# Kernel optimization log

Measured on AMD Instinct MI355X. Metric: run time of the kernel, lower is better.

Reference implementation:

```python
import jax, jax.numpy as jnp
import numpy as np

WH, WW = 7, 7
N = WH * WW
H = 16          # num_heads
D = 32          # head_dim
NW = 64         # num windows per image (mask.shape[0])


def _relative_position_index(wh, ww):
    coords = np.stack(np.meshgrid(np.arange(wh), np.arange(ww), indexing='ij'))  # (2, wh, ww)
    cf = coords.reshape(2, -1)                                                   # (2, N)
    rel = cf[:, :, None] - cf[:, None, :]                                        # (2, N, N)
    rel = rel.transpose(1, 2, 0).copy()
    rel[:, :, 0] += wh - 1
    rel[:, :, 1] += ww - 1
    rel[:, :, 0] *= 2 * ww - 1
    return rel.sum(-1)  # (N, N) int

REL_IDX = jnp.asarray(_relative_position_index(WH, WW))


def setup_inputs() -> dict:
    key = jax.random.key(0)
    ks = jax.random.split(key, 5)
    B_ = 2048
    dim = H * D
    x = jax.random.normal(ks[0], (B_, N, dim), dtype=jnp.float32)
    mask = jnp.zeros((NW, N, N), dtype=jnp.float32)
    rpb_table = jax.random.normal(ks[1], ((2 * WH - 1) * (2 * WW - 1), H), dtype=jnp.float32) * 0.02
    qkv_w = jax.random.normal(ks[2], (3 * dim, dim), dtype=jnp.float32) * (dim ** -0.5)
    qkv_b = jnp.zeros((3 * dim,), dtype=jnp.float32)
    proj_w = jax.random.normal(ks[3], (dim, dim), dtype=jnp.float32) * (dim ** -0.5)
    proj_b = jnp.zeros((dim,), dtype=jnp.float32)
    return {"x": x, "mask": mask, "rpb_table": rpb_table,
            "qkv_w": qkv_w, "qkv_b": qkv_b, "proj_w": proj_w, "proj_b": proj_b}


def reference(x, mask, rpb_table, qkv_w, qkv_b, proj_w, proj_b):
    B_, n, C = x.shape
    scale = D ** -0.5
    # qkv projection (torch Linear: x @ W^T + b)
    qkv = (x @ qkv_w.T + qkv_b).reshape(B_, n, 3, H, D)
    q = qkv[:, :, 0].transpose(0, 2, 1, 3) * scale  # (B_, H, N, D)
    k = qkv[:, :, 1].transpose(0, 2, 1, 3)
    v = qkv[:, :, 2].transpose(0, 2, 1, 3)
    attn = jnp.einsum('bhnd,bhmd->bhnm', q, k)      # (B_, H, N, N)
    # relative position bias: gather (N*N,) rows from table -> (N, N, H) -> (H, N, N)
    bias = rpb_table[REL_IDX.reshape(-1)].reshape(n, n, H).transpose(2, 0, 1)
    attn = attn + bias[None]
    # shifted-window mask add: (B, nW, H, N, N) + (1, nW, 1, N, N)
    nW = mask.shape[0]
    attn = attn.reshape(B_ // nW, nW, H, n, n) + mask[None, :, None]
    attn = attn.reshape(B_, H, n, n)
    attn = jax.nn.softmax(attn, axis=-1)
    out = jnp.einsum('bhnm,bhmd->bhnd', attn, v)    # (B_, H, N, D)
    out = out.transpose(0, 2, 1, 3).reshape(B_, n, H * D)
    return out @ proj_w.T + proj_b
```

## Files before the change

### kernel.cpp

```cpp
#include <hip/hip_runtime.h>

typedef _Float16 f16;
typedef _Float16 f16x8 __attribute__((ext_vector_type(8)));
typedef _Float16 f16x4 __attribute__((ext_vector_type(4)));
typedef float f32x4 __attribute__((ext_vector_type(4)));

#define NTOK 49
#define NH 16
#define HD 32
#define DIM 512
#define NWIN 64
#define NB 2048
#define MTOT (NB*NTOK)
#define SCALE 0.17677669529663687f
#define VTS 56

__device__ __forceinline__ void gload_lds16(const f16* g, f16* l) {
    __builtin_amdgcn_global_load_lds((const __attribute__((address_space(1))) void*)g,
                                     (__attribute__((address_space(3))) void*)l, 16, 0, 0);
}

__global__ __launch_bounds__(256) void cvt_f32_f16(const float* __restrict__ s,
                                                   f16* __restrict__ d, int n4) {
    int i = blockIdx.x * 256 + threadIdx.x;
    int st = gridDim.x * 256;
    for (; i < n4; i += st) {
        float4 v = ((const float4*)s)[i];
        f16x4 o = { (f16)v.x, (f16)v.y, (f16)v.z, (f16)v.w };
        *(f16x4*)(d + (size_t)i * 4) = o;
    }
}

__global__ __launch_bounds__(256) void build_comb2(const float* __restrict__ rpb,
                                                   const float* __restrict__ mask,
                                                   float* __restrict__ comb2) {
    int idx = blockIdx.x * 256 + threadIdx.x;
    int r4   = idx & 3;
    int tj   = (idx >> 2) & 3;
    int ti   = (idx >> 4) & 3;
    int lane = (idx >> 6) & 63;
    int wh   = idx >> 12;
    int h = wh & 15, w = wh >> 4;
    int g = lane >> 4, c16 = lane & 15;
    int row = ti * 16 + g * 4 + r4;
    int col = tj * 16 + c16;
    float v = 0.f;
    if (row < NTOK && col < NTOK) {
        int ri = row / 7, ci = row - ri * 7;
        int rj = col / 7, cj = col - rj * 7;
        int rel = (ri - rj + 6) * 13 + (ci - cj + 6);
        v = rpb[rel * NH + h] + mask[(w * NTOK + row) * NTOK + col];
    }
    comb2[idx] = v;
}

template<int MODE, int NT>
__global__ __launch_bounds__(256, 3) void gemm_kernel(const f16* __restrict__ A,
                                                      const f16* __restrict__ Bw,
                                                      const float* __restrict__ bias,
                                                      f16* __restrict__ qo,
                                                      f16* __restrict__ ko,
                                                      f16* __restrict__ vto,
                                                      float* __restrict__ outp) {
    __shared__ __align__(16) f16 As[3][128][32];
    __shared__ __align__(16) f16 Bs[3][128][32];

    const int tid = threadIdx.x;
    const int lane = tid & 63;
    const int wv = tid >> 6;
    const int wr = wv >> 1, wc = wv & 1;
    const int g = lane >> 4, c16 = lane & 15;
    const int rsw = (c16 >> 1) & 3;

    const int nblk = gridDim.x;
    const int f = blockIdx.x;
    const int work = (f & 7) * (nblk >> 3) + (f >> 3);
    const int m0 = (work / NT) * 128;
    const int n0 = (work % NT) * 128;

    const int srow = lane >> 2;
    const int schunk = (lane & 3) ^ ((srow >> 1) & 3);
    const f16* gA = A  + (size_t)(m0 + wv * 32 + srow) * DIM + schunk * 8;
    const f16* gB = Bw + (size_t)(n0 + wv * 32 + srow) * DIM + schunk * 8;

#define STAGE(buf, t) do { \
    gload_lds16(gA + (t) * 32,                     &As[buf][wv * 32][0]);      \
    gload_lds16(gA + (size_t)16 * DIM + (t) * 32,  &As[buf][wv * 32 + 16][0]); \
    gload_lds16(gB + (t) * 32,                     &Bs[buf][wv * 32][0]);      \
    gload_lds16(gB + (size_t)16 * DIM + (t) * 32,  &Bs[buf][wv * 32 + 16][0]); \
} while (0)

    f32x4 acc[4][4];
#pragma unroll
    for (int j = 0; j < 4; ++j)
#pragma unroll
        for (int i = 0; i < 4; ++i)
            acc[j][i] = (f32x4){0.f, 0.f, 0.f, 0.f};

    STAGE(0, 0);
    STAGE(1, 1);
    asm volatile("s_waitcnt vmcnt(4)" ::: "memory");
    __builtin_amdgcn_s_barrier();

    const int KS = DIM / 32;
#pragma unroll
    for (int t = 0; t < KS; ++t) {
        const int cb = t % 3;
        if (t + 2 < KS) STAGE((t + 2) % 3, t + 2);
        f16x8 af[4], bf[4];
#pragma unroll
        for (int i = 0; i < 4; ++i)
            af[i] = *(const f16x8*)&As[cb][wr * 64 + i * 16 + c16][(g ^ rsw) * 8];
#pragma unroll
        for (int j = 0; j < 4; ++j)
            bf[j] = *(const f16x8*)&Bs[cb][wc * 64 + j * 16 + c16][(g ^ rsw) * 8];
        __builtin_amdgcn_s_setprio(1);
#pragma unroll
        for (int j = 0; j < 4; ++j)
#pragma unroll
            for (int i = 0; i < 4; ++i)
                acc[j][i] = __builtin_amdgcn_mfma_f32_16x16x32_f16(bf[j], af[i], acc[j][i], 0, 0, 0);
        __builtin_amdgcn_s_setprio(0);
        asm volatile("s_waitcnt lgkmcnt(0)" ::: "memory");
        __builtin_amdgcn_sched_barrier(0);
        if (t + 2 < KS) {
            asm volatile("s_waitcnt vmcnt(4)" ::: "memory");
        } else if (t + 1 < KS) {
            asm volatile("s_waitcnt vmcnt(0)" ::: "memory");
        }
        if (t + 1 < KS) __builtin_amdgcn_s_barrier();
    }
#undef STAGE

#pragma unroll
    for (int i = 0; i < 4; ++i) {
        const int m = m0 + wr * 64 + i * 16 + c16;
        int b = 0, tk = 0;
        if (MODE == 0) { b = m / NTOK; tk = m - b * NTOK; }
#pragma unroll
        for (int j = 0; j < 4; ++j) {
            const int n = n0 + wc * 64 + j * 16 + g * 4;
            f32x4 v = acc[j][i];
            const f32x4 b4 = *(const f32x4*)&bias[n];
            v += b4;
            if (MODE == 0) {
                const int s = n >> 9;
                const int hh = (n >> 5) & 15;
                const int d0 = n & 31;
                const size_t bh = (size_t)(b * NH + hh);
                if (s == 0) {
                    f16x4 o = { (f16)(v[0] * SCALE), (f16)(v[1] * SCALE),
                                (f16)(v[2] * SCALE), (f16)(v[3] * SCALE) };
                    *(f16x4*)(qo + (bh * NTOK + tk) * HD + d0) = o;
                } else if (s == 1) {
                    f16x4 o = { (f16)v[0], (f16)v[1], (f16)v[2], (f16)v[3] };
                    *(f16x4*)(ko + (bh * NTOK + tk) * HD + d0) = o;
                } else {
#pragma unroll
                    for (int r = 0; r < 4; ++r)
                        vto[(bh * HD + d0 + r) * VTS + tk] = (f16)v[r];
                }
            } else {
                float4 o = { v[0], v[1], v[2], v[3] };
                *(float4*)(outp + (size_t)m * DIM + n) = o;
            }
        }
    }
}

__global__ __launch_bounds__(256) void attn_kernel(const f16* __restrict__ qw,
                                                   const f16* __restrict__ kw,
                                                   const f16* __restrict__ vt,
                                                   const float* __restrict__ comb2,
                                                   f16* __restrict__ aout) {
    __shared__ __align__(16) f16 Ps[4][64][72];

    const int wv = threadIdx.x >> 6;
    const int l = threadIdx.x & 63;
    const int f = blockIdx.x;
    const int work = (f & 7) * (gridDim.x >> 3) + (f >> 3);
    const int bid = work * 4 + wv;
    const int b = bid >> 4, h = bid & 15;
    const int w = b & (NWIN - 1);
    const int g = l >> 4, c16 = l & 15;
    const size_t qkbase = (size_t)bid * (NTOK * HD);
    const size_t vbase = (size_t)bid * (HD * VTS);

    const f16x8 z8 = {};

    f16x8 qf[4], kf[4];
#pragma unroll
    for (int t = 0; t < 4; ++t) {
        int row = t * 16 + c16;
        f16x8 q = z8, k = z8;
        if (row < NTOK) {
            q = *(const f16x8*)(qw + qkbase + row * HD + g * 8);
            k = *(const f16x8*)(kw + qkbase + row * HD + g * 8);
        }
        qf[t] = q; kf[t] = k;
    }

    const float* cb = comb2 + (((size_t)(w * NH + h) * 64 + l) << 6);
    f32x4 S[4][4];
#pragma unroll
    for (int i = 0; i < 4; ++i)
#pragma unroll
        for (int j = 0; j < 4; ++j)
            S[i][j] = *(const f32x4*)(cb + (i * 4 + j) * 4);
#pragma unroll
    for (int i = 0; i < 4; ++i)
#pragma unroll
        for (int j = 0; j < 4; ++j)
            S[i][j] = __builtin_amdgcn_mfma_f32_16x16x32_f16(qf[i], kf[j], S[i][j], 0, 0, 0);

#pragma unroll
    for (int ti = 0; ti < 4; ++ti)
#pragma unroll
        for (int r = 0; r < 4; ++r) {
            int row = ti * 16 + g * 4 + r;
            float v0 = S[ti][0][r], v1 = S[ti][1][r], v2 = S[ti][2][r];
            float v3 = (c16 == 0) ? S[ti][3][r] : -1e30f;
            float mx = fmaxf(fmaxf(v0, v1), fmaxf(v2, v3));
#pragma unroll
            for (int mk = 1; mk < 16; mk <<= 1) mx = fmaxf(mx, __shfl_xor(mx, mk, 64));
            float p0 = __expf(v0 - mx), p1 = __expf(v1 - mx), p2 = __expf(v2 - mx);
            float p3 = (c16 == 0) ? __expf(v3 - mx) : 0.f;
            float sm = p0 + p1 + p2 + p3;
#pragma unroll
            for (int mk = 1; mk < 16; mk <<= 1) sm += __shfl_xor(sm, mk, 64);
            float inv = 1.f / sm;
            Ps[wv][row][c16]      = (f16)(p0 * inv);
            Ps[wv][row][16 + c16] = (f16)(p1 * inv);
            Ps[wv][row][32 + c16] = (f16)(p2 * inv);
            Ps[wv][row][48 + c16] = (f16)(p3 * inv);
        }
    __syncthreads();

    f32x4 O[4][2];
    const f32x4 zf = (f32x4){0.f, 0.f, 0.f, 0.f};
#pragma unroll
    for (int i = 0; i < 4; ++i) { O[i][0] = zf; O[i][1] = zf; }
#pragma unroll
    for (int c = 0; c < 2; ++c) {
        f16x8 pf[4], vf[2];
#pragma unroll
        for (int ti = 0; ti < 4; ++ti)
            pf[ti] = *(const f16x8*)&Ps[wv][ti * 16 + c16][c * 32 + g * 8];
        int tcol = c * 32 + g * 8;
#pragma unroll
        for (int td = 0; td < 2; ++td) {
            f16x8 vv = z8;
            if (tcol < VTS)
                vv = *(const f16x8*)(vt + vbase + (size_t)(td * 16 + c16) * VTS + tcol);
            vf[td] = vv;
        }
#pragma unroll
        for (int ti = 0; ti < 4; ++ti)
#pragma unroll
            for (int td = 0; td < 2; ++td)
                O[ti][td] = __builtin_amdgcn_mfma_f32_16x16x32_f16(pf[ti], vf[td], O[ti][td], 0, 0, 0);
    }

#pragma unroll
    for (int ti = 0; ti < 4; ++ti)
#pragma unroll
        for (int r = 0; r < 4; ++r) {
            int row = ti * 16 + g * 4 + r;
            if (row < NTOK) {
                size_t ob = ((size_t)(b * NTOK + row)) * DIM + h * HD;
                aout[ob + c16]      = (f16)O[ti][0][r];
                aout[ob + 16 + c16] = (f16)O[ti][1][r];
            }
        }
}

extern "C" void kernel_launch(void* const* d_in, const int* in_sizes, int n_in,
                              void* d_out, int out_size, void* d_ws, size_t ws_size,
                              hipStream_t stream) {
    const float* x      = (const float*)d_in[0];
    const float* mask   = (const float*)d_in[1];
    const float* rpb    = (const float*)d_in[2];
    const float* qkv_w  = (const float*)d_in[3];
    const float* qkv_b  = (const float*)d_in[4];
    const float* proj_w = (const float*)d_in[5];
    const float* proj_b = (const float*)d_in[6];
    float* out = (float*)d_out;

    char* ws = (char*)d_ws;
    size_t o = 0;
    f16* x16   = (f16*)(ws + o); o += (size_t)MTOT * DIM * 2;
    f16* w16   = (f16*)(ws + o); o += (size_t)1536 * 512 * 2;
    f16* pw16  = (f16*)(ws + o); o += (size_t)512 * 512 * 2;
    f16* qws   = (f16*)(ws + o); o += (size_t)NB * NH * NTOK * HD * 2;
    f16* kws   = (f16*)(ws + o); o += (size_t)NB * NH * NTOK * HD * 2;
    f16* vtws  = (f16*)(ws + o); o += (size_t)NB * NH * HD * VTS * 2;
    float* cb2 = (float*)(ws + o);
    f16* aout = x16;

    cvt_f32_f16<<<dim3(2048), dim3(256), 0, stream>>>(x, x16, MTOT * DIM / 4);
    cvt_f32_f16<<<dim3(768), dim3(256), 0, stream>>>(qkv_w, w16, 1536 * 512 / 4);
    cvt_f32_f16<<<dim3(256), dim3(256), 0, stream>>>(proj_w, pw16, 512 * 512 / 4);

    build_comb2<<<dim3(16384), dim3(256), 0, stream>>>(rpb, mask, cb2);

    gemm_kernel<0, 12><<<dim3((MTOT / 128) * 12), dim3(256), 0, stream>>>(
        x16, w16, qkv_b, qws, kws, vtws, nullptr);

    attn_kernel<<<dim3(NB * NH / 4), dim3(256), 0, stream>>>(qws, kws, vtws, cb2, aout);

    gemm_kernel<1, 4><<<dim3((MTOT / 128) * 4), dim3(256), 0, stream>>>(
        aout, pw16, proj_b, nullptr, nullptr, nullptr, out);
}
```

Baseline: 604.5 us.

## Enlarge GEMM tiles to 256x256 with 8 waves, fp16 bias table, transposed PV output

The GEMM moves from 128x128 tiles with 256 threads and a 3-stage pipeline to 256x256 tiles with 512 threads and a 4-stage LDS pipeline, cutting global reloads of A and B per output. The combined bias/mask table is stored in fp16 to halve its read traffic in attention. The PV MFMA operand order is swapped so each lane writes contiguous f16x4 output instead of scattered scalars. Larger tiles raise register and LDS use (128 KB LDS, launch bounds of one block per CU), which can reduce occupancy and latency hiding, and fp16 bias adds slight rounding.

```diff
diff --git a/kernel.cpp b/kernel.cpp
--- a/kernel.cpp
+++ b/kernel.cpp
@@ -33,7 +33,7 @@
 
 __global__ __launch_bounds__(256) void build_comb2(const float* __restrict__ rpb,
                                                    const float* __restrict__ mask,
-                                                   float* __restrict__ comb2) {
+                                                   f16* __restrict__ comb2) {
     int idx = blockIdx.x * 256 + threadIdx.x;
     int r4   = idx & 3;
     int tj   = (idx >> 2) & 3;
@@ -51,79 +51,81 @@
         int rel = (ri - rj + 6) * 13 + (ci - cj + 6);
         v = rpb[rel * NH + h] + mask[(w * NTOK + row) * NTOK + col];
     }
-    comb2[idx] = v;
+    comb2[idx] = (f16)v;
 }
 
 template<int MODE, int NT>
-__global__ __launch_bounds__(256, 3) void gemm_kernel(const f16* __restrict__ A,
+__global__ __launch_bounds__(512, 1) void gemm_kernel(const f16* __restrict__ A,
                                                       const f16* __restrict__ Bw,
                                                       const float* __restrict__ bias,
                                                       f16* __restrict__ qo,
                                                       f16* __restrict__ ko,
                                                       f16* __restrict__ vto,
                                                       float* __restrict__ outp) {
-    __shared__ __align__(16) f16 As[3][128][32];
-    __shared__ __align__(16) f16 Bs[3][128][32];
+    __shared__ __align__(16) f16 As[4][256][32];
+    __shared__ __align__(16) f16 Bs[4][256][32];
 
     const int tid = threadIdx.x;
     const int lane = tid & 63;
     const int wv = tid >> 6;
-    const int wr = wv >> 1, wc = wv & 1;
+    const int wm = wv >> 2, wn = wv & 3;
     const int g = lane >> 4, c16 = lane & 15;
     const int rsw = (c16 >> 1) & 3;
 
     const int nblk = gridDim.x;
     const int f = blockIdx.x;
     const int work = (f & 7) * (nblk >> 3) + (f >> 3);
-    const int m0 = (work / NT) * 128;
-    const int n0 = (work % NT) * 128;
+    const int m0 = (work / NT) * 256;
+    const int n0 = (work % NT) * 256;
 
     const int srow = lane >> 2;
     const int schunk = (lane & 3) ^ ((srow >> 1) & 3);
-    const f16* gA = A  + (size_t)(m0 + wv * 32 + srow) * DIM + schunk * 8;
-    const f16* gB = Bw + (size_t)(n0 + wv * 32 + srow) * DIM + schunk * 8;
-
-#define STAGE(buf, t) do { \
-    gload_lds16(gA + (t) * 32,                     &As[buf][wv * 32][0]);      \
-    gload_lds16(gA + (size_t)16 * DIM + (t) * 32,  &As[buf][wv * 32 + 16][0]); \
-    gload_lds16(gB + (t) * 32,                     &Bs[buf][wv * 32][0]);      \
-    gload_lds16(gB + (size_t)16 * DIM + (t) * 32,  &Bs[buf][wv * 32 + 16][0]); \
-} while (0)
-
-    f32x4 acc[4][4];
+    const f16* gAlo = A  + (size_t)(m0 + wv * 16 + srow) * DIM + schunk * 8;
+    const f16* gAhi = gAlo + (size_t)128 * DIM;
+    const f16* gBlo = Bw + (size_t)(n0 + wv * 16 + srow) * DIM + schunk * 8;
+    const f16* gBhi = gBlo + (size_t)128 * DIM;
+
+#define STAGE(t) do { const int _b = (t) & 3; const int _k = (t) * 32;     \
+    gload_lds16(gAlo + _k, &As[_b][wv * 16][0]);                           \
+    gload_lds16(gAhi + _k, &As[_b][128 + wv * 16][0]);                     \
+    gload_lds16(gBlo + _k, &Bs[_b][wv * 16][0]);                           \
+    gload_lds16(gBhi + _k, &Bs[_b][128 + wv * 16][0]); } while (0)
+
+    f32x4 acc[4][8];
 #pragma unroll
     for (int j = 0; j < 4; ++j)
 #pragma unroll
-        for (int i = 0; i < 4; ++i)
+        for (int i = 0; i < 8; ++i)
             acc[j][i] = (f32x4){0.f, 0.f, 0.f, 0.f};
 
-    STAGE(0, 0);
-    STAGE(1, 1);
-    asm volatile("s_waitcnt vmcnt(4)" ::: "memory");
+    STAGE(0); STAGE(1); STAGE(2);
+    asm volatile("s_waitcnt vmcnt(8)" ::: "memory");
     __builtin_amdgcn_s_barrier();
 
     const int KS = DIM / 32;
 #pragma unroll
     for (int t = 0; t < KS; ++t) {
-        const int cb = t % 3;
-        if (t + 2 < KS) STAGE((t + 2) % 3, t + 2);
-        f16x8 af[4], bf[4];
-#pragma unroll
-        for (int i = 0; i < 4; ++i)
-            af[i] = *(const f16x8*)&As[cb][wr * 64 + i * 16 + c16][(g ^ rsw) * 8];
+        const int cb = t & 3;
+        if (t + 3 < KS) STAGE(t + 3);
+        f16x8 af[8], bf[4];
+#pragma unroll
+        for (int i = 0; i < 8; ++i)
+            af[i] = *(const f16x8*)&As[cb][wm * 128 + i * 16 + c16][(g ^ rsw) * 8];
 #pragma unroll
         for (int j = 0; j < 4; ++j)
-            bf[j] = *(const f16x8*)&Bs[cb][wc * 64 + j * 16 + c16][(g ^ rsw) * 8];
+            bf[j] = *(const f16x8*)&Bs[cb][wn * 64 + j * 16 + c16][(g ^ rsw) * 8];
         __builtin_amdgcn_s_setprio(1);
 #pragma unroll
         for (int j = 0; j < 4; ++j)
 #pragma unroll
-            for (int i = 0; i < 4; ++i)
+            for (int i = 0; i < 8; ++i)
                 acc[j][i] = __builtin_amdgcn_mfma_f32_16x16x32_f16(bf[j], af[i], acc[j][i], 0, 0, 0);
         __builtin_amdgcn_s_setprio(0);
         asm volatile("s_waitcnt lgkmcnt(0)" ::: "memory");
         __builtin_amdgcn_sched_barrier(0);
-        if (t + 2 < KS) {
+        if (t + 3 < KS) {
+            asm volatile("s_waitcnt vmcnt(8)" ::: "memory");
+        } else if (t + 2 < KS) {
             asm volatile("s_waitcnt vmcnt(4)" ::: "memory");
         } else if (t + 1 < KS) {
             asm volatile("s_waitcnt vmcnt(0)" ::: "memory");
@@ -133,13 +135,13 @@
 #undef STAGE
 
 #pragma unroll
-    for (int i = 0; i < 4; ++i) {
-        const int m = m0 + wr * 64 + i * 16 + c16;
+    for (int i = 0; i < 8; ++i) {
+        const int m = m0 + wm * 128 + i * 16 + c16;
         int b = 0, tk = 0;
         if (MODE == 0) { b = m / NTOK; tk = m - b * NTOK; }
 #pragma unroll
         for (int j = 0; j < 4; ++j) {
-            const int n = n0 + wc * 64 + j * 16 + g * 4;
+            const int n = n0 + wn * 64 + j * 16 + g * 4;
             f32x4 v = acc[j][i];
             const f32x4 b4 = *(const f32x4*)&bias[n];
             v += b4;
@@ -171,7 +173,7 @@
 __global__ __launch_bounds__(256) void attn_kernel(const f16* __restrict__ qw,
                                                    const f16* __restrict__ kw,
                                                    const f16* __restrict__ vt,
-                                                   const float* __restrict__ comb2,
+                                                   const f16* __restrict__ comb2,
                                                    f16* __restrict__ aout) {
     __shared__ __align__(16) f16 Ps[4][64][72];
 
@@ -200,13 +202,20 @@
         qf[t] = q; kf[t] = k;
     }
 
-    const float* cb = comb2 + (((size_t)(w * NH + h) * 64 + l) << 6);
+    const f16* cb = comb2 + (((size_t)(w * NH + h) * 64 + l) << 6);
+    f16x8 cbv[8];
+#pragma unroll
+    for (int k = 0; k < 8; ++k) cbv[k] = *(const f16x8*)(cb + k * 8);
     f32x4 S[4][4];
 #pragma unroll
     for (int i = 0; i < 4; ++i)
 #pragma unroll
-        for (int j = 0; j < 4; ++j)
-            S[i][j] = *(const f32x4*)(cb + (i * 4 + j) * 4);
+        for (int j = 0; j < 4; ++j) {
+            const int e = i * 16 + j * 4;
+#pragma unroll
+            for (int r = 0; r < 4; ++r)
+                S[i][j][r] = (float)cbv[(e + r) >> 3][(e + r) & 7];
+        }
 #pragma unroll
     for (int i = 0; i < 4; ++i)
 #pragma unroll
@@ -236,10 +245,12 @@
         }
     __syncthreads();
 
-    f32x4 O[4][2];
+    f32x4 O2[2][4];
     const f32x4 zf = (f32x4){0.f, 0.f, 0.f, 0.f};
 #pragma unroll
-    for (int i = 0; i < 4; ++i) { O[i][0] = zf; O[i][1] = zf; }
+    for (int td = 0; td < 2; ++td)
+#pragma unroll
+        for (int ti = 0; ti < 4; ++ti) O2[td][ti] = zf;
 #pragma unroll
     for (int c = 0; c < 2; ++c) {
         f16x8 pf[4], vf[2];
@@ -255,23 +266,25 @@
             vf[td] = vv;
         }
 #pragma unroll
-        for (int ti = 0; ti < 4; ++ti)
-#pragma unroll
-            for (int td = 0; td < 2; ++td)
-                O[ti][td] = __builtin_amdgcn_mfma_f32_16x16x32_f16(pf[ti], vf[td], O[ti][td], 0, 0, 0);
-    }
-
-#pragma unroll
-    for (int ti = 0; ti < 4; ++ti)
-#pragma unroll
-        for (int r = 0; r < 4; ++r) {
-            int row = ti * 16 + g * 4 + r;
-            if (row < NTOK) {
-                size_t ob = ((size_t)(b * NTOK + row)) * DIM + h * HD;
-                aout[ob + c16]      = (f16)O[ti][0][r];
-                aout[ob + 16 + c16] = (f16)O[ti][1][r];
+        for (int td = 0; td < 2; ++td)
+#pragma unroll
+            for (int ti = 0; ti < 4; ++ti)
+                O2[td][ti] = __builtin_amdgcn_mfma_f32_16x16x32_f16(vf[td], pf[ti], O2[td][ti], 0, 0, 0);
+    }
+
+#pragma unroll
+    for (int ti = 0; ti < 4; ++ti) {
+        int tok = ti * 16 + c16;
+        if (tok < NTOK) {
+            size_t ob = ((size_t)(b * NTOK + tok)) * DIM + h * HD;
+#pragma unroll
+            for (int td = 0; td < 2; ++td) {
+                f32x4 v = O2[td][ti];
+                f16x4 o = { (f16)v[0], (f16)v[1], (f16)v[2], (f16)v[3] };
+                *(f16x4*)(aout + ob + td * 16 + g * 4) = o;
             }
         }
+    }
 }
 
 extern "C" void kernel_launch(void* const* d_in, const int* in_sizes, int n_in,
@@ -294,7 +307,7 @@
     f16* qws   = (f16*)(ws + o); o += (size_t)NB * NH * NTOK * HD * 2;
     f16* kws   = (f16*)(ws + o); o += (size_t)NB * NH * NTOK * HD * 2;
     f16* vtws  = (f16*)(ws + o); o += (size_t)NB * NH * HD * VTS * 2;
-    float* cb2 = (float*)(ws + o);
+    f16* cb2   = (f16*)(ws + o);
     f16* aout = x16;
 
     cvt_f32_f16<<<dim3(2048), dim3(256), 0, stream>>>(x, x16, MTOT * DIM / 4);
@@ -303,11 +316,11 @@
 
     build_comb2<<<dim3(16384), dim3(256), 0, stream>>>(rpb, mask, cb2);
 
-    gemm_kernel<0, 12><<<dim3((MTOT / 128) * 12), dim3(256), 0, stream>>>(
+    gemm_kernel<0, 6><<<dim3((MTOT / 256) * 6), dim3(512), 0, stream>>>(
         x16, w16, qkv_b, qws, kws, vtws, nullptr);
 
     attn_kernel<<<dim3(NB * NH / 4), dim3(256), 0, stream>>>(qws, kws, vtws, cb2, aout);
 
-    gemm_kernel<1, 4><<<dim3((MTOT / 128) * 4), dim3(256), 0, stream>>>(
+    gemm_kernel<1, 2><<<dim3((MTOT / 256) * 2), dim3(512), 0, stream>>>(
         aout, pw16, proj_b, nullptr, nullptr, nullptr, out);
 }
```

Measured after the change: 579.5 us. 1.04x faster.
